# Optimization experiments

Measured on AMD Instinct MI355X. Metric: run time of the kernel, lower is better.

## Reference

```python
import jax, jax.numpy as jnp
import numpy as np

D_MODEL = 1024
NUM_HEADS = 16
D_HEAD = D_MODEL // NUM_HEADS
BATCH = 4
SEQ = 2048
NEG_INF = -1e30


def setup_inputs() -> dict:
    key = jax.random.key(0)
    k_x, k_q, k_k, k_v, k_o = jax.random.split(key, 5)
    scale = 1.0 / np.sqrt(D_MODEL)
    x = jax.random.normal(k_x, (BATCH, SEQ, D_MODEL), dtype=jnp.float32)
    Qw = jax.random.normal(k_q, (D_MODEL, D_MODEL), dtype=jnp.float32) * scale
    Kw = jax.random.normal(k_k, (D_MODEL, D_MODEL), dtype=jnp.float32) * scale
    Vw = jax.random.normal(k_v, (D_MODEL, D_MODEL), dtype=jnp.float32) * scale
    Ow = jax.random.normal(k_o, (D_MODEL, D_MODEL), dtype=jnp.float32) * scale
    padding_mask = jnp.zeros((BATCH, SEQ), dtype=bool)  # True = masked position
    return {"x": x, "Qw": Qw, "Kw": Kw, "Vw": Vw, "Ow": Ow, "padding_mask": padding_mask}


def reference(x, Qw, Kw, Vw, Ow, padding_mask):
    B, S, D = x.shape
    H, dh = NUM_HEADS, D_HEAD
    # torch Linear (no bias): y = x @ W.T
    q = jnp.einsum("bsd,ed->bse", x, Qw).reshape(B, S, H, dh)
    k = jnp.einsum("bsd,ed->bse", x, Kw).reshape(B, S, H, dh)
    v = jnp.einsum("bsd,ed->bse", x, Vw).reshape(B, S, H, dh)
    # scores: [B, H, Sq, Sk]
    score = jnp.einsum("bqhd,bkhd->bhqk", q, k) / jnp.sqrt(jnp.float32(dh))
    # causal mask (masked=True)
    causal = jnp.tril(jnp.ones((S, S), dtype=bool))  # True = keep
    score = jnp.where(causal[None, None, :, :], score, NEG_INF)
    # padding mask: True = masked key position
    score = jnp.where(padding_mask[:, None, None, :], NEG_INF, score)
    attn = jax.nn.softmax(score, axis=-1)  # dropout=0.0 (eval mode)
    ctx = jnp.einsum("bhqk,bkhd->bqhd", attn, v).reshape(B, S, D)
    out = jnp.einsum("bsd,ed->bse", ctx, Ow)
    return out
```

## Files before the change

### kernel.cpp

```cpp
#include <hip/hip_runtime.h>
#include <hip/hip_bf16.h>

typedef __attribute__((ext_vector_type(8))) short short8;
typedef __attribute__((ext_vector_type(4))) float f32x4;

#define MFMA_BF16_16x16x32(a,b,c) __builtin_amdgcn_mfma_f32_16x16x32_bf16((a),(b),(c),0,0,0)

constexpr int B_  = 4;
constexpr int S_  = 2048;
constexpr int H_  = 16;
constexpr int DH_ = 64;
constexpr int D_  = 1024;
constexpr int M_  = B_ * S_;

__device__ __forceinline__ unsigned short f2bf(float f) {
  union { float f; unsigned u; } v; v.f = f;
  unsigned u = v.u;
  u += 0x7fffu + ((u >> 16) & 1u);
  return (unsigned short)(u >> 16);
}

__device__ __forceinline__ short8 cvt8(f32x4 a, f32x4 b) {
  union { __hip_bfloat162 h[4]; short8 s; } u;
  u.h[0] = __float22bfloat162_rn(make_float2(a[0], a[1]));
  u.h[1] = __float22bfloat162_rn(make_float2(a[2], a[3]));
  u.h[2] = __float22bfloat162_rn(make_float2(b[0], b[1]));
  u.h[3] = __float22bfloat162_rn(make_float2(b[2], b[3]));
  return u.s;
}

__device__ __forceinline__ unsigned pk2(float a, float b) {
  union { __hip_bfloat162 h; unsigned u; } z;
  z.h = __float22bfloat162_rn(make_float2(a, b));
  return z.u;
}

__global__ __launch_bounds__(256)
void cvt_x(const float* __restrict__ x, unsigned short* __restrict__ xb) {
  const size_t i = ((size_t)blockIdx.x * 256 + threadIdx.x) * 8;
  f32x4 a = *(const f32x4*)(x + i);
  f32x4 b = *(const f32x4*)(x + i + 4);
  *(short8*)(xb + i) = cvt8(a, b);
}

__global__ __launch_bounds__(256)
void gemm_qkv(const unsigned short* __restrict__ xb,
              const float* __restrict__ Qw, const float* __restrict__ Kw,
              const float* __restrict__ Vw,
              unsigned short* __restrict__ Qo, unsigned short* __restrict__ Ko,
              unsigned short* __restrict__ VTo) {
  constexpr int BM = 128, BK = 32, LDK = 40;
  __shared__ __align__(16) short As[BM * LDK];
  __shared__ __align__(16) short Bs[BM * LDK];

  const int nb = blockIdx.x;
  const float* W;
  unsigned short* out;
  float scale = 1.0f;
  int epi;
  if (nb < 8)       { W = Qw; out = Qo;  scale = 0.125f; epi = 1; }
  else if (nb < 16) { W = Kw; out = Ko;  epi = 1; }
  else              { W = Vw; out = VTo; epi = 2; }

  const int tid  = threadIdx.x;
  const int lane = tid & 63;
  const int w    = tid >> 6;
  const int quad = lane >> 4;
  const int l16  = lane & 15;
  const int wm   = (w >> 1) * 64;
  const int wn   = (w & 1) * 64;

  const int m0 = blockIdx.y * BM;
  const int n0 = (nb & 7) * 128;

  f32x4 acc[4][4];
  #pragma unroll
  for (int i = 0; i < 4; ++i)
    #pragma unroll
    for (int j = 0; j < 4; ++j)
      acc[i][j] = (f32x4){0.f, 0.f, 0.f, 0.f};

  for (int k0 = 0; k0 < D_; k0 += BK) {
    __syncthreads();
    #pragma unroll
    for (int i = 0; i < 2; ++i) {
      int flat = i * 256 + tid;
      int row  = flat >> 2;
      int col  = (flat & 3) * 8;
      *(short8*)(&As[row * LDK + col]) =
          *(const short8*)(xb + (size_t)(m0 + row) * D_ + k0 + col);
      const float* Wp = W + (size_t)(n0 + row) * D_ + k0 + col;
      *(short8*)(&Bs[row * LDK + col]) = cvt8(*(const f32x4*)Wp, *(const f32x4*)(Wp + 4));
    }
    __syncthreads();

    short8 af[4], bf[4];
    #pragma unroll
    for (int i = 0; i < 4; ++i)
      af[i] = *(const short8*)(&As[(wm + i * 16 + l16) * LDK + quad * 8]);
    #pragma unroll
    for (int j = 0; j < 4; ++j)
      bf[j] = *(const short8*)(&Bs[(wn + j * 16 + l16) * LDK + quad * 8]);
    #pragma unroll
    for (int i = 0; i < 4; ++i)
      #pragma unroll
      for (int j = 0; j < 4; ++j)
        acc[i][j] = MFMA_BF16_16x16x32(af[i], bf[j], acc[i][j]);
  }

  #pragma unroll
  for (int i = 0; i < 4; ++i)
    #pragma unroll
    for (int j = 0; j < 4; ++j)
      #pragma unroll
      for (int r = 0; r < 4; ++r) {
        int m = m0 + wm + i * 16 + quad * 4 + r;
        int n = n0 + wn + j * 16 + l16;
        unsigned short bv = f2bf(acc[i][j][r] * scale);
        int b = m >> 11, s = m & (S_ - 1);
        int h = n >> 6,  d = n & (DH_ - 1);
        if (epi == 1)
          out[((size_t)(b * H_ + h) * S_ + s) * DH_ + d] = bv;
        else
          out[((size_t)(b * H_ + h) * DH_ + d) * S_ + s] = bv;
      }
}

__global__ __launch_bounds__(256)
void gemm_out(const unsigned short* __restrict__ A,
              const float* __restrict__ W,
              float* __restrict__ out) {
  constexpr int BM = 128, BK = 32, LDK = 40;
  __shared__ __align__(16) short As[BM * LDK];
  __shared__ __align__(16) short Bs[BM * LDK];

  const int tid  = threadIdx.x;
  const int lane = tid & 63;
  const int w    = tid >> 6;
  const int quad = lane >> 4;
  const int l16  = lane & 15;
  const int wm   = (w >> 1) * 64;
  const int wn   = (w & 1) * 64;

  const int m0 = blockIdx.y * BM;
  const int n0 = blockIdx.x * 128;

  f32x4 acc[4][4];
  #pragma unroll
  for (int i = 0; i < 4; ++i)
    #pragma unroll
    for (int j = 0; j < 4; ++j)
      acc[i][j] = (f32x4){0.f, 0.f, 0.f, 0.f};

  for (int k0 = 0; k0 < D_; k0 += BK) {
    __syncthreads();
    #pragma unroll
    for (int i = 0; i < 2; ++i) {
      int flat = i * 256 + tid;
      int row  = flat >> 2;
      int col  = (flat & 3) * 8;
      *(short8*)(&As[row * LDK + col]) =
          *(const short8*)(A + (size_t)(m0 + row) * D_ + k0 + col);
      const float* Wp = W + (size_t)(n0 + row) * D_ + k0 + col;
      *(short8*)(&Bs[row * LDK + col]) = cvt8(*(const f32x4*)Wp, *(const f32x4*)(Wp + 4));
    }
    __syncthreads();

    short8 af[4], bf[4];
    #pragma unroll
    for (int i = 0; i < 4; ++i)
      af[i] = *(const short8*)(&As[(wm + i * 16 + l16) * LDK + quad * 8]);
    #pragma unroll
    for (int j = 0; j < 4; ++j)
      bf[j] = *(const short8*)(&Bs[(wn + j * 16 + l16) * LDK + quad * 8]);
    #pragma unroll
    for (int i = 0; i < 4; ++i)
      #pragma unroll
      for (int j = 0; j < 4; ++j)
        acc[i][j] = MFMA_BF16_16x16x32(af[i], bf[j], acc[i][j]);
  }

  #pragma unroll
  for (int i = 0; i < 4; ++i)
    #pragma unroll
    for (int j = 0; j < 4; ++j)
      #pragma unroll
      for (int r = 0; r < 4; ++r) {
        int m = m0 + wm + i * 16 + quad * 4 + r;
        int n = n0 + wn + j * 16 + l16;
        out[(size_t)m * D_ + n] = acc[i][j][r];
      }
}

constexpr int LDP_ = 72;

__device__ __forceinline__ void attn_range(
    const unsigned short* __restrict__ Kh,
    const unsigned short* __restrict__ Vh,
    const unsigned char* __restrict__ pmb,
    short* __restrict__ Pw,
    const short8 qf[2][2], f32x4 acc[2][4], f32x4 lacc[2],
    int qw, int kt0, int kt1, int quad, int l16) {
  const short8 ones = {0x3F80, 0x3F80, 0x3F80, 0x3F80,
                       0x3F80, 0x3F80, 0x3F80, 0x3F80};
  for (int kt = kt0; kt < kt1; ++kt) {
    const int k0 = kt * 64;

    short8 kb[8];
    #pragma unroll
    for (int t = 0; t < 4; ++t) {
      const unsigned short* kp = Kh + (size_t)(k0 + t * 16 + l16) * DH_ + quad * 8;
      kb[t * 2]     = *(const short8*)(kp);
      kb[t * 2 + 1] = *(const short8*)(kp + 32);
    }
    unsigned pm4[4];
    #pragma unroll
    for (int t = 0; t < 4; ++t)
      pm4[t] = *(const unsigned*)(pmb + k0 + t * 16 + quad * 4);

    f32x4 sc[2][4];
    __builtin_amdgcn_s_setprio(1);
    #pragma unroll
    for (int t = 0; t < 4; ++t) {
      #pragma unroll
      for (int i = 0; i < 2; ++i) {
        f32x4 z = (f32x4){0.f, 0.f, 0.f, 0.f};
        z = MFMA_BF16_16x16x32(kb[t * 2], qf[i][0], z);
        sc[i][t] = MFMA_BF16_16x16x32(kb[t * 2 + 1], qf[i][1], z);
      }
    }
    __builtin_amdgcn_s_setprio(0);

    short8 vb[8];
    #pragma unroll
    for (int t = 0; t < 4; ++t)
      vb[t] = *(const short8*)(Vh + (size_t)(t * 16 + l16) * S_ + k0 + quad * 8);

    #pragma unroll
    for (int i = 0; i < 2; ++i)
      #pragma unroll
      for (int t = 0; t < 4; ++t)
        #pragma unroll
        for (int r = 0; r < 4; ++r) {
          float e = __expf(sc[i][t][r]);
          sc[i][t][r] = ((pm4[t] >> (8 * r)) & 0xffu) ? 0.f : e;
        }
    if (k0 + 63 > qw) {
      #pragma unroll
      for (int t = 0; t < 4; ++t)
        #pragma unroll
        for (int r = 0; r < 4; ++r) {
          int key = k0 + t * 16 + quad * 4 + r;
          #pragma unroll
          for (int i = 0; i < 2; ++i) {
            int qrow = qw + i * 16 + l16;
            if (key > qrow) sc[i][t][r] = 0.f;
          }
        }
    }

    #pragma unroll
    for (int i = 0; i < 2; ++i)
      #pragma unroll
      for (int t = 0; t < 4; ++t) {
        unsigned lo = pk2(sc[i][t][0], sc[i][t][1]);
        unsigned hi = pk2(sc[i][t][2], sc[i][t][3]);
        *(uint2*)(&Pw[(i * 16 + l16) * LDP_ + t * 16 + quad * 4]) = make_uint2(lo, hi);
      }

    #pragma unroll
    for (int t = 0; t < 4; ++t)
      vb[4 + t] = *(const short8*)(Vh + (size_t)(t * 16 + l16) * S_ + k0 + 32 + quad * 8);

    __builtin_amdgcn_s_setprio(1);
    #pragma unroll
    for (int ks = 0; ks < 2; ++ks) {
      short8 pa0 = *(const short8*)(&Pw[l16 * LDP_ + ks * 32 + quad * 8]);
      short8 pa1 = *(const short8*)(&Pw[(16 + l16) * LDP_ + ks * 32 + quad * 8]);
      #pragma unroll
      for (int t = 0; t < 4; ++t) {
        acc[0][t] = MFMA_BF16_16x16x32(pa0, vb[ks * 4 + t], acc[0][t]);
        acc[1][t] = MFMA_BF16_16x16x32(pa1, vb[ks * 4 + t], acc[1][t]);
      }
      lacc[0] = MFMA_BF16_16x16x32(pa0, ones, lacc[0]);
      lacc[1] = MFMA_BF16_16x16x32(pa1, ones, lacc[1]);
    }
    __builtin_amdgcn_s_setprio(0);
  }
}

__global__ __launch_bounds__(128)
void attn(const unsigned short* __restrict__ Q,
          const unsigned short* __restrict__ K,
          const unsigned short* __restrict__ VT,
          const unsigned char* __restrict__ pmask,
          unsigned short* __restrict__ CTX) {
  __shared__ __align__(16) short Ps[2 * 32 * LDP_];
  __shared__ float Rbuf[64 * 40];

  const int tid  = threadIdx.x;
  const int lane = tid & 63;
  const int w    = tid >> 6;
  const int quad = lane >> 4;
  const int l16  = lane & 15;

  const int L    = blockIdx.x;
  const int xcd  = L & 7;
  const int slot = L >> 3;
  const int bh   = xcd + 8 * (slot & 7);
  const int p    = slot >> 3;
  const int b    = bh >> 4;
  const int h    = bh & 15;

  const int qtA = p, qtB = 63 - p;
  const int ntA = (qtA >> 1) + 1;
  const int ntB = (qtB >> 1) + 1;
  const int splitB = 17 - ntA;

  const unsigned short* Qh = Q  + ((size_t)b * H_ + h) * S_ * DH_;
  const unsigned short* Kh = K  + ((size_t)b * H_ + h) * S_ * DH_;
  const unsigned short* Vh = VT + ((size_t)b * H_ + h) * DH_ * S_;
  const unsigned char* pmb = pmask + (size_t)b * S_;
  unsigned short* CTXb = CTX + (size_t)b * S_ * D_;
  short* Pw = &Ps[w * 32 * LDP_];

  f32x4 acc[2][4];
  f32x4 lacc[2];
  short8 qf[2][2];

  if (w == 0) {
    {
      const int qw = qtA * 32;
      #pragma unroll
      for (int i = 0; i < 2; ++i)
        #pragma unroll
        for (int c = 0; c < 2; ++c)
          qf[i][c] = *(const short8*)(Qh + (size_t)(qw + i * 16 + l16) * DH_ + c * 32 + quad * 8);
      #pragma unroll
      for (int i = 0; i < 2; ++i) {
        #pragma unroll
        for (int t = 0; t < 4; ++t) acc[i][t] = (f32x4){0.f, 0.f, 0.f, 0.f};
        lacc[i] = (f32x4){0.f, 0.f, 0.f, 0.f};
      }
      attn_range(Kh, Vh, pmb, Pw, qf, acc, lacc, qw, 0, ntA, quad, l16);
      #pragma unroll
      for (int i = 0; i < 2; ++i)
        #pragma unroll
        for (int r = 0; r < 4; ++r) {
          int qrow = qw + i * 16 + quad * 4 + r;
          float inv = 1.0f / lacc[i][r];
          #pragma unroll
          for (int t = 0; t < 4; ++t)
            CTXb[(size_t)qrow * D_ + h * DH_ + t * 16 + l16] = f2bf(acc[i][t][r] * inv);
        }
    }
    {
      const int qw = qtB * 32;
      #pragma unroll
      for (int i = 0; i < 2; ++i)
        #pragma unroll
        for (int c = 0; c < 2; ++c)
          qf[i][c] = *(const short8*)(Qh + (size_t)(qw + i * 16 + l16) * DH_ + c * 32 + quad * 8);
      #pragma unroll
      for (int i = 0; i < 2; ++i) {
        #pragma unroll
        for (int t = 0; t < 4; ++t) acc[i][t] = (f32x4){0.f, 0.f, 0.f, 0.f};
        lacc[i] = (f32x4){0.f, 0.f, 0.f, 0.f};
      }
      attn_range(Kh, Vh, pmb, Pw, qf, acc, lacc, qw, 0, splitB, quad, l16);
      __syncthreads();
      #pragma unroll
      for (int i = 0; i < 2; ++i) {
        #pragma unroll
        for (int t = 0; t < 4; ++t)
          #pragma unroll
          for (int r = 0; r < 4; ++r)
            acc[i][t][r] += Rbuf[lane * 40 + i * 16 + t * 4 + r];
        #pragma unroll
        for (int r = 0; r < 4; ++r)
          lacc[i][r] += Rbuf[lane * 40 + 32 + i * 4 + r];
      }
      #pragma unroll
      for (int i = 0; i < 2; ++i)
        #pragma unroll
        for (int r = 0; r < 4; ++r) {
          int qrow = qw + i * 16 + quad * 4 + r;
          float inv = 1.0f / lacc[i][r];
          #pragma unroll
          for (int t = 0; t < 4; ++t)
            CTXb[(size_t)qrow * D_ + h * DH_ + t * 16 + l16] = f2bf(acc[i][t][r] * inv);
        }
    }
  } else {
    const int qw = qtB * 32;
    #pragma unroll
    for (int i = 0; i < 2; ++i)
      #pragma unroll
      for (int c = 0; c < 2; ++c)
        qf[i][c] = *(const short8*)(Qh + (size_t)(qw + i * 16 + l16) * DH_ + c * 32 + quad * 8);
    #pragma unroll
    for (int i = 0; i < 2; ++i) {
      #pragma unroll
      for (int t = 0; t < 4; ++t) acc[i][t] = (f32x4){0.f, 0.f, 0.f, 0.f};
      lacc[i] = (f32x4){0.f, 0.f, 0.f, 0.f};
    }
    attn_range(Kh, Vh, pmb, Pw, qf, acc, lacc, qw, splitB, ntB, quad, l16);
    #pragma unroll
    for (int i = 0; i < 2; ++i) {
      #pragma unroll
      for (int t = 0; t < 4; ++t)
        #pragma unroll
        for (int r = 0; r < 4; ++r)
          Rbuf[lane * 40 + i * 16 + t * 4 + r] = acc[i][t][r];
      #pragma unroll
      for (int r = 0; r < 4; ++r)
        Rbuf[lane * 40 + 32 + i * 4 + r] = lacc[i][r];
    }
    __syncthreads();
  }
}

extern "C" void kernel_launch(void* const* d_in, const int* in_sizes, int n_in,
                              void* d_out, int out_size, void* d_ws, size_t ws_size,
                              hipStream_t stream) {
  const float* x  = (const float*)d_in[0];
  const float* Qw = (const float*)d_in[1];
  const float* Kw = (const float*)d_in[2];
  const float* Vw = (const float*)d_in[3];
  const float* Ow = (const float*)d_in[4];
  const unsigned char* pm = (const unsigned char*)d_in[5];

  const size_t NE = (size_t)M_ * D_;
  unsigned short* Qall  = (unsigned short*)d_out;
  unsigned short* CTXa  = (unsigned short*)d_out + NE;
  unsigned short* Kall  = (unsigned short*)d_ws;
  unsigned short* VTall = (unsigned short*)d_ws + NE;

  cvt_x<<<dim3((M_ * D_) / (256 * 8)), 256, 0, stream>>>(x, CTXa);

  gemm_qkv<<<dim3(24, M_ / 128), 256, 0, stream>>>(CTXa, Qw, Kw, Vw,
                                                   Qall, Kall, VTall);

  attn<<<dim3(2048), 128, 0, stream>>>(Qall, Kall, VTall, pm, CTXa);

  hipMemcpyAsync(d_ws, (const void*)CTXa, NE * sizeof(unsigned short),
                 hipMemcpyDeviceToDevice, stream);

  gemm_out<<<dim3(D_ / 128, M_ / 128), 256, 0, stream>>>((unsigned short*)d_ws,
                                                         Ow, (float*)d_out);
}
```

Baseline: 373.7 us.

## Pre-convert weights to bf16 and stage GEMM tiles via direct global-to-LDS loads

Weights are converted to bf16 once in a separate pass instead of being converted from fp32 inside every GEMM tile load. The bf16 GEMMs then stage A and B tiles with the global_load_lds builtin straight into unpadded LDS. This cuts redundant weight reads and per-tile conversion work. In exchange it adds extra launches and workspace, needs a fallback path when workspace is small, and the unpadded LDS stride may cause bank conflicts on fragment reads.

```diff
diff --git a/kernel.cpp b/kernel.cpp
--- a/kernel.cpp
+++ b/kernel.cpp
@@ -38,29 +38,49 @@
 __global__ __launch_bounds__(256)
 void cvt_x(const float* __restrict__ x, unsigned short* __restrict__ xb) {
   const size_t i = ((size_t)blockIdx.x * 256 + threadIdx.x) * 8;
-  f32x4 a = *(const f32x4*)(x + i);
-  f32x4 b = *(const f32x4*)(x + i + 4);
-  *(short8*)(xb + i) = cvt8(a, b);
+  *(short8*)(xb + i) = cvt8(*(const f32x4*)(x + i), *(const f32x4*)(x + i + 4));
 }
 
 __global__ __launch_bounds__(256)
-void gemm_qkv(const unsigned short* __restrict__ xb,
-              const float* __restrict__ Qw, const float* __restrict__ Kw,
-              const float* __restrict__ Vw,
-              unsigned short* __restrict__ Qo, unsigned short* __restrict__ Ko,
-              unsigned short* __restrict__ VTo) {
-  constexpr int BM = 128, BK = 32, LDK = 40;
-  __shared__ __align__(16) short As[BM * LDK];
-  __shared__ __align__(16) short Bs[BM * LDK];
-
-  const int nb = blockIdx.x;
-  const float* W;
-  unsigned short* out;
-  float scale = 1.0f;
-  int epi;
-  if (nb < 8)       { W = Qw; out = Qo;  scale = 0.125f; epi = 1; }
-  else if (nb < 16) { W = Kw; out = Ko;  epi = 1; }
-  else              { W = Vw; out = VTo; epi = 2; }
+void cvt_w(const float* __restrict__ s0, const float* __restrict__ s1,
+           const float* __restrict__ s2,
+           unsigned short* __restrict__ d0, unsigned short* __restrict__ d1,
+           unsigned short* __restrict__ d2) {
+  const int a = blockIdx.x >> 9;
+  const float* s = (a == 0) ? s0 : (a == 1) ? s1 : s2;
+  unsigned short* d = (a == 0) ? d0 : (a == 1) ? d1 : d2;
+  const size_t i = ((size_t)(blockIdx.x & 511) * 256 + threadIdx.x) * 8;
+  *(short8*)(d + i) = cvt8(*(const f32x4*)(s + i), *(const f32x4*)(s + i + 4));
+}
+
+__device__ __forceinline__ void stage16(const unsigned short* __restrict__ g,
+                                        short* lds_wave_base, int lane) {
+#if __has_builtin(__builtin_amdgcn_global_load_lds)
+  __builtin_amdgcn_global_load_lds(
+      (const __attribute__((address_space(1))) unsigned int*)g,
+      (__attribute__((address_space(3))) unsigned int*)lds_wave_base, 16, 0, 0);
+#else
+  *(short8*)(lds_wave_base + lane * 8) = *(const short8*)g;
+#endif
+}
+
+__global__ __launch_bounds__(256)
+void gemm_bb(const unsigned short* __restrict__ xb,
+             const unsigned short* __restrict__ Qwb,
+             const unsigned short* __restrict__ Kwb,
+             const unsigned short* __restrict__ Vwb,
+             unsigned short* __restrict__ Qo, unsigned short* __restrict__ Ko,
+             unsigned short* __restrict__ VTo, int haveQ) {
+  __shared__ __align__(16) short As[128 * 32];
+  __shared__ __align__(16) short Bs[128 * 32];
+
+  const int nb  = blockIdx.x;
+  const int sel = haveQ ? (nb >> 3) : 1 + (nb >> 3);
+  const int n0  = (nb & 7) * 128;
+  const unsigned short* Wb = (sel == 0) ? Qwb : (sel == 1) ? Kwb : Vwb;
+  unsigned short* out      = (sel == 0) ? Qo  : (sel == 1) ? Ko  : VTo;
+  const float scale = (sel == 0) ? 0.125f : 1.0f;
+  const int epi = (sel == 2) ? 2 : 1;
 
   const int tid  = threadIdx.x;
   const int lane = tid & 63;
@@ -69,9 +89,10 @@
   const int l16  = lane & 15;
   const int wm   = (w >> 1) * 64;
   const int wn   = (w & 1) * 64;
-
-  const int m0 = blockIdx.y * BM;
-  const int n0 = (nb & 7) * 128;
+  const int m0   = blockIdx.y * 128;
+
+  const int srow = tid >> 2;
+  const int scol = (tid & 3) * 8;
 
   f32x4 acc[4][4];
   #pragma unroll
@@ -80,27 +101,23 @@
     for (int j = 0; j < 4; ++j)
       acc[i][j] = (f32x4){0.f, 0.f, 0.f, 0.f};
 
-  for (int k0 = 0; k0 < D_; k0 += BK) {
-    __syncthreads();
-    #pragma unroll
-    for (int i = 0; i < 2; ++i) {
-      int flat = i * 256 + tid;
-      int row  = flat >> 2;
-      int col  = (flat & 3) * 8;
-      *(short8*)(&As[row * LDK + col]) =
-          *(const short8*)(xb + (size_t)(m0 + row) * D_ + k0 + col);
-      const float* Wp = W + (size_t)(n0 + row) * D_ + k0 + col;
-      *(short8*)(&Bs[row * LDK + col]) = cvt8(*(const f32x4*)Wp, *(const f32x4*)(Wp + 4));
+  for (int k0 = 0; k0 < D_; k0 += 32) {
+    __syncthreads();
+    #pragma unroll
+    for (int j = 0; j < 2; ++j) {
+      const int row = j * 64 + srow;
+      stage16(xb + (size_t)(m0 + row) * D_ + k0 + scol, As + j * 2048 + w * 512, lane);
+      stage16(Wb + (size_t)(n0 + row) * D_ + k0 + scol, Bs + j * 2048 + w * 512, lane);
     }
     __syncthreads();
 
     short8 af[4], bf[4];
     #pragma unroll
     for (int i = 0; i < 4; ++i)
-      af[i] = *(const short8*)(&As[(wm + i * 16 + l16) * LDK + quad * 8]);
-    #pragma unroll
-    for (int j = 0; j < 4; ++j)
-      bf[j] = *(const short8*)(&Bs[(wn + j * 16 + l16) * LDK + quad * 8]);
+      af[i] = *(const short8*)(&As[(wm + i * 16 + l16) * 32 + quad * 8]);
+    #pragma unroll
+    for (int j = 0; j < 4; ++j)
+      bf[j] = *(const short8*)(&Bs[(wn + j * 16 + l16) * 32 + quad * 8]);
     #pragma unroll
     for (int i = 0; i < 4; ++i)
       #pragma unroll
@@ -127,12 +144,11 @@
 }
 
 __global__ __launch_bounds__(256)
-void gemm_out(const unsigned short* __restrict__ A,
-              const float* __restrict__ W,
-              float* __restrict__ out) {
-  constexpr int BM = 128, BK = 32, LDK = 40;
-  __shared__ __align__(16) short As[BM * LDK];
-  __shared__ __align__(16) short Bs[BM * LDK];
+void gemm_out_bb(const unsigned short* __restrict__ A,
+                 const unsigned short* __restrict__ Wb,
+                 float* __restrict__ out) {
+  __shared__ __align__(16) short As[128 * 32];
+  __shared__ __align__(16) short Bs[128 * 32];
 
   const int tid  = threadIdx.x;
   const int lane = tid & 63;
@@ -141,9 +157,11 @@
   const int l16  = lane & 15;
   const int wm   = (w >> 1) * 64;
   const int wn   = (w & 1) * 64;
-
-  const int m0 = blockIdx.y * BM;
-  const int n0 = blockIdx.x * 128;
+  const int m0   = blockIdx.y * 128;
+  const int n0   = blockIdx.x * 128;
+
+  const int srow = tid >> 2;
+  const int scol = (tid & 3) * 8;
 
   f32x4 acc[4][4];
   #pragma unroll
@@ -152,7 +170,68 @@
     for (int j = 0; j < 4; ++j)
       acc[i][j] = (f32x4){0.f, 0.f, 0.f, 0.f};
 
-  for (int k0 = 0; k0 < D_; k0 += BK) {
+  for (int k0 = 0; k0 < D_; k0 += 32) {
+    __syncthreads();
+    #pragma unroll
+    for (int j = 0; j < 2; ++j) {
+      const int row = j * 64 + srow;
+      stage16(A  + (size_t)(m0 + row) * D_ + k0 + scol, As + j * 2048 + w * 512, lane);
+      stage16(Wb + (size_t)(n0 + row) * D_ + k0 + scol, Bs + j * 2048 + w * 512, lane);
+    }
+    __syncthreads();
+
+    short8 af[4], bf[4];
+    #pragma unroll
+    for (int i = 0; i < 4; ++i)
+      af[i] = *(const short8*)(&As[(wm + i * 16 + l16) * 32 + quad * 8]);
+    #pragma unroll
+    for (int j = 0; j < 4; ++j)
+      bf[j] = *(const short8*)(&Bs[(wn + j * 16 + l16) * 32 + quad * 8]);
+    #pragma unroll
+    for (int i = 0; i < 4; ++i)
+      #pragma unroll
+      for (int j = 0; j < 4; ++j)
+        acc[i][j] = MFMA_BF16_16x16x32(af[i], bf[j], acc[i][j]);
+  }
+
+  #pragma unroll
+  for (int i = 0; i < 4; ++i)
+    #pragma unroll
+    for (int j = 0; j < 4; ++j)
+      #pragma unroll
+      for (int r = 0; r < 4; ++r) {
+        int m = m0 + wm + i * 16 + quad * 4 + r;
+        int n = n0 + wn + j * 16 + l16;
+        out[(size_t)m * D_ + n] = acc[i][j][r];
+      }
+}
+
+__global__ __launch_bounds__(256)
+void gemm_q_f32w(const unsigned short* __restrict__ xb,
+                 const float* __restrict__ Qw,
+                 unsigned short* __restrict__ Qo) {
+  constexpr int LDK = 40;
+  __shared__ __align__(16) short As[128 * LDK];
+  __shared__ __align__(16) short Bs[128 * LDK];
+
+  const int tid  = threadIdx.x;
+  const int lane = tid & 63;
+  const int w    = tid >> 6;
+  const int quad = lane >> 4;
+  const int l16  = lane & 15;
+  const int wm   = (w >> 1) * 64;
+  const int wn   = (w & 1) * 64;
+  const int m0   = blockIdx.y * 128;
+  const int n0   = blockIdx.x * 128;
+
+  f32x4 acc[4][4];
+  #pragma unroll
+  for (int i = 0; i < 4; ++i)
+    #pragma unroll
+    for (int j = 0; j < 4; ++j)
+      acc[i][j] = (f32x4){0.f, 0.f, 0.f, 0.f};
+
+  for (int k0 = 0; k0 < D_; k0 += 32) {
     __syncthreads();
     #pragma unroll
     for (int i = 0; i < 2; ++i) {
@@ -160,8 +239,8 @@
       int row  = flat >> 2;
       int col  = (flat & 3) * 8;
       *(short8*)(&As[row * LDK + col]) =
-          *(const short8*)(A + (size_t)(m0 + row) * D_ + k0 + col);
-      const float* Wp = W + (size_t)(n0 + row) * D_ + k0 + col;
+          *(const short8*)(xb + (size_t)(m0 + row) * D_ + k0 + col);
+      const float* Wp = Qw + (size_t)(n0 + row) * D_ + k0 + col;
       *(short8*)(&Bs[row * LDK + col]) = cvt8(*(const f32x4*)Wp, *(const f32x4*)(Wp + 4));
     }
     __syncthreads();
@@ -188,7 +267,10 @@
       for (int r = 0; r < 4; ++r) {
         int m = m0 + wm + i * 16 + quad * 4 + r;
         int n = n0 + wn + j * 16 + l16;
-        out[(size_t)m * D_ + n] = acc[i][j][r];
+        unsigned short bv = f2bf(acc[i][j][r] * 0.125f);
+        int b = m >> 11, s = m & (S_ - 1);
+        int h = n >> 6,  d = n & (DH_ - 1);
+        Qo[((size_t)(b * H_ + h) * S_ + s) * DH_ + d] = bv;
       }
 }
 
@@ -431,21 +513,41 @@
   const unsigned char* pm = (const unsigned char*)d_in[5];
 
   const size_t NE = (size_t)M_ * D_;
+  const size_t DD = (size_t)D_ * D_;
   unsigned short* Qall  = (unsigned short*)d_out;
   unsigned short* CTXa  = (unsigned short*)d_out + NE;
-  unsigned short* Kall  = (unsigned short*)d_ws;
-  unsigned short* VTall = (unsigned short*)d_ws + NE;
-
-  cvt_x<<<dim3((M_ * D_) / (256 * 8)), 256, 0, stream>>>(x, CTXa);
-
-  gemm_qkv<<<dim3(24, M_ / 128), 256, 0, stream>>>(CTXa, Qw, Kw, Vw,
-                                                   Qall, Kall, VTall);
+  unsigned short* ws16  = (unsigned short*)d_ws;
+  unsigned short* Kall  = ws16;
+  unsigned short* VTall = ws16 + NE;
+  unsigned short* Owb   = VTall;
+
+  const bool tail = ws_size >= (2 * NE + 3 * DD) * sizeof(unsigned short);
+
+  cvt_x<<<dim3((unsigned)(NE / 2048)), 256, 0, stream>>>(x, CTXa);
+
+  if (tail) {
+    unsigned short* Qwb = ws16 + 2 * NE;
+    unsigned short* Kwb = Qwb + DD;
+    unsigned short* Vwb = Kwb + DD;
+    cvt_w<<<dim3(3 * 512), 256, 0, stream>>>(Qw, Kw, Vw, Qwb, Kwb, Vwb);
+    gemm_bb<<<dim3(24, M_ / 128), 256, 0, stream>>>(CTXa, Qwb, Kwb, Vwb,
+                                                    Qall, Kall, VTall, 1);
+  } else {
+    unsigned short* Kwb = Qall;
+    unsigned short* Vwb = Qall + DD;
+    cvt_w<<<dim3(2 * 512), 256, 0, stream>>>(Kw, Vw, Vw, Kwb, Vwb, Vwb);
+    gemm_bb<<<dim3(16, M_ / 128), 256, 0, stream>>>(CTXa, nullptr, Kwb, Vwb,
+                                                    Qall, Kall, VTall, 0);
+    gemm_q_f32w<<<dim3(8, M_ / 128), 256, 0, stream>>>(CTXa, Qw, Qall);
+  }
 
   attn<<<dim3(2048), 128, 0, stream>>>(Qall, Kall, VTall, pm, CTXa);
+
+  cvt_w<<<dim3(512), 256, 0, stream>>>(Ow, Ow, Ow, Owb, Owb, Owb);
 
   hipMemcpyAsync(d_ws, (const void*)CTXa, NE * sizeof(unsigned short),
                  hipMemcpyDeviceToDevice, stream);
 
-  gemm_out<<<dim3(D_ / 128, M_ / 128), 256, 0, stream>>>((unsigned short*)d_ws,
-                                                         Ow, (float*)d_out);
-}
+  gemm_out_bb<<<dim3(D_ / 128, M_ / 128), 256, 0, stream>>>(ws16, Owb,
+                                                            (float*)d_out);
+}
```

After: 349.7 us. 6.4% less time.
